# Kernel tuning notes

Measured on AMD Instinct MI355X. Metric: run time of the kernel, lower is better.

## Reference

```python
import jax, jax.numpy as jnp
import numpy as np

B, T, C, HS = 4, 2048, 1024, 64

def setup_inputs() -> dict:
    key = jax.random.key(0)
    k1, k2, k3, k4 = jax.random.split(key, 4)
    x = jax.random.normal(k1, (B, T, C), dtype=jnp.float32)
    # torch Linear default init scale ~ 1/sqrt(fan_in); scale weights similarly
    s = C ** -0.5
    Wq = jax.random.normal(k2, (C, HS), dtype=jnp.float32) * s
    Wk = jax.random.normal(k3, (C, HS), dtype=jnp.float32) * s
    Wv = jax.random.normal(k4, (C, HS), dtype=jnp.float32) * s
    return {"x": x, "Wq": Wq, "Wk": Wk, "Wv": Wv}

def reference(x, Wq, Wk, Wv):
    B_, T_, C_ = x.shape
    q = x @ Wq          # [B,T,HS]
    k = x @ Wk          # [B,T,HS]
    v = x @ Wv          # [B,T,HS]
    scale = C_ ** -0.5  # note: module scales by input dim C, not head_size
    w = jnp.einsum('bqh,bkh->bqk', q, k) * scale  # [B,T,T]
    causal = jnp.tril(jnp.ones((T_, T_), dtype=bool))
    w = jnp.where(causal, w, -jnp.inf)
    a = jax.nn.softmax(w, axis=-1)  # dropout is identity (eval / drop_rate=0)
    return jnp.einsum('bqk,bkh->bqh', a, v)
```

## Files before the change

kernel.cpp:

```cpp
#include <hip/hip_runtime.h>
#include <math.h>

#define B_  4
#define T_  2048
#define C_  1024
#define HS_ 64
#define M_  (B_*T_)
#define NCAT 192
#define SCALE_ 0.03125f
#define XPAD 1032

typedef unsigned short ushort_t;
typedef short bf16x8 __attribute__((ext_vector_type(8)));
typedef float f32x4 __attribute__((ext_vector_type(4)));

static __device__ __forceinline__ unsigned short f2bf(float f) {
    union { float f; unsigned int u; } c; c.f = f;
    unsigned int u = c.u;
    return (unsigned short)((u + 0x7FFFu + ((u >> 16) & 1u)) >> 16);
}
static __device__ __forceinline__ unsigned short f2bf_fast(float f) {
    union { float f; unsigned int u; } c; c.f = f;
    return (unsigned short)((c.u + 0x8000u) >> 16);
}

__global__ void wconv_kernel(const float* __restrict__ Wq, const float* __restrict__ Wk,
                             const float* __restrict__ Wv, ushort_t* __restrict__ wtp) {
    int l = threadIdx.x & 63;
    int g = blockIdx.x * 4 + (threadIdx.x >> 6);
    int c  = g / 12;
    int nt = g % 12;
    const float* W = (nt < 4) ? Wq : (nt < 8) ? Wk : Wv;
    int nn = (nt & 3) * 16 + (l & 15);
    int k0 = c * 32 + (l >> 4) * 8;
    union { bf16x8 v; ushort_t u[8]; } pk;
    #pragma unroll
    for (int e = 0; e < 8; e++)
        pk.u[e] = f2bf(W[(size_t)(k0 + e) * HS_ + nn]);
    *(bf16x8*)(wtp + ((size_t)g * 64 + l) * 8) = pk.v;
}

__global__ __launch_bounds__(512, 4) void proj_kernel(const float* __restrict__ x,
    const ushort_t* __restrict__ wtp,
    ushort_t* __restrict__ qws, ushort_t* __restrict__ kws, ushort_t* __restrict__ vt) {
    __shared__ __align__(16) unsigned char pool[49152];

    int tid  = threadIdx.x;
    int wid  = tid >> 6;
    int lane = tid & 63;
    int qd   = lane >> 4;
    int lq   = lane & 15;
    int r0   = blockIdx.x * 16;

    ushort_t* xs = (ushort_t*)pool;
    {
        float4 xv[8];
        #pragma unroll
        for (int j = 0; j < 8; j++) {
            int flat4 = j * 512 + tid;
            int row   = flat4 >> 8;
            int c4    = flat4 & 255;
            xv[j] = *(const float4*)(x + (size_t)(r0 + row) * C_ + c4 * 4);
        }
        #pragma unroll
        for (int j = 0; j < 8; j++) {
            int flat4 = j * 512 + tid;
            int row   = flat4 >> 8;
            int c4    = flat4 & 255;
            uint2 p;
            p.x = (unsigned)f2bf(xv[j].x) | ((unsigned)f2bf(xv[j].y) << 16);
            p.y = (unsigned)f2bf(xv[j].z) | ((unsigned)f2bf(xv[j].w) << 16);
            *(uint2*)(xs + row * XPAD + c4 * 4) = p;
        }
    }
    __syncthreads();

    f32x4 acc[12];
    #pragma unroll
    for (int i = 0; i < 12; i++) acc[i] = (f32x4){0.f,0.f,0.f,0.f};

    const ushort_t* xrow = xs + lq * XPAD + wid * 128 + qd * 8;
    #pragma unroll
    for (int i = 0; i < 4; i++) {
        bf16x8 af = *(const bf16x8*)(xrow + i * 32);
        #pragma unroll
        for (int nt = 0; nt < 12; nt++) {
            bf16x8 bv = *(const bf16x8*)(wtp +
                (((size_t)(wid * 4 + i) * 12 + nt) * 64 + lane) * 8);
            acc[nt] = __builtin_amdgcn_mfma_f32_16x16x32_bf16(af, bv, acc[nt], 0, 0, 0);
        }
    }

    __syncthreads();
    f32x4 (*red)[12 * 64] = (f32x4 (*)[12 * 64])pool;
    if (wid >= 4) {
        #pragma unroll
        for (int nt = 0; nt < 12; nt++) red[wid - 4][nt * 64 + lane] = acc[nt];
    }
    __syncthreads();
    if (wid < 4) {
        #pragma unroll
        for (int nt = 0; nt < 12; nt++) acc[nt] += red[wid][nt * 64 + lane];
    }
    __syncthreads();
    if (wid == 2 || wid == 3) {
        #pragma unroll
        for (int nt = 0; nt < 12; nt++) red[wid][nt * 64 + lane] = acc[nt];
    }
    __syncthreads();
    if (wid < 2) {
        #pragma unroll
        for (int nt = 0; nt < 12; nt++) acc[nt] += red[wid + 2][nt * 64 + lane];
    }
    __syncthreads();
    if (wid == 1) {
        #pragma unroll
        for (int nt = 0; nt < 12; nt++) red[0][nt * 64 + lane] = acc[nt];
    }
    __syncthreads();
    if (wid == 0) {
        #pragma unroll
        for (int nt = 0; nt < 12; nt++) {
            acc[nt] += red[0][nt * 64 + lane];
            int outn = nt >> 2;
            int col  = (nt & 3) * 16 + lq;
            #pragma unroll
            for (int r = 0; r < 4; r++) {
                int row = r0 + qd * 4 + r;
                float v = acc[nt][r];
                if (outn == 0) v *= SCALE_;
                ushort_t val = f2bf(v);
                if (outn == 0)      qws[(size_t)row * HS_ + col] = val;
                else if (outn == 1) kws[(size_t)row * HS_ + col] = val;
                else {
                    int b = row >> 11, t = row & 2047;
                    vt[((size_t)b * 64 + col) * T_ + t] = val;
                }
            }
        }
    }
}

__global__ __launch_bounds__(512, 2) void flash_kernel(const ushort_t* __restrict__ qws,
    const ushort_t* __restrict__ kws, const ushort_t* __restrict__ vt,
    float* __restrict__ out) {
    __shared__ __align__(16) unsigned char pool[18432];

    int tid  = threadIdx.x;
    int wid  = tid >> 6;
    int lane = tid & 63;
    int qd   = lane >> 4;
    int lq   = lane & 15;
    int ts   = wid >> 2;
    int ws   = wid & 3;

    int batch = blockIdx.y;
    int p     = blockIdx.x;
    int tile  = ts ? (127 - p) : p;
    int q0    = tile * 16;
    int qrow  = q0 + lq;
    int grow  = batch * T_ + qrow;
    int nU    = (tile + 4) >> 2;

    bf16x8 qf[2];
    #pragma unroll
    for (int st = 0; st < 2; st++)
        qf[st] = *(const bf16x8*)(qws + (size_t)grow * HS_ + st * 32 + qd * 8);

    float lsum = 0.f;
    f32x4 O[4];
    #pragma unroll
    for (int nt = 0; nt < 4; nt++) O[nt] = (f32x4){0.f,0.f,0.f,0.f};

    ushort_t* pw = (ushort_t*)pool + wid * 1152 + lq * 72;
    const ushort_t* kp    = kws + (size_t)batch * T_ * HS_;
    const ushort_t* vbase = vt  + (size_t)batch * 64 * T_;

    for (int u = ws; u < nU; u += 4) {
        int kb = u * 64;

        bf16x8 kf[8], vf[8];
        #pragma unroll
        for (int sub = 0; sub < 4; sub++)
            #pragma unroll
            for (int st = 0; st < 2; st++)
                kf[sub * 2 + st] = *(const bf16x8*)(kp + (size_t)(kb + sub * 16 + lq) * HS_ + st * 32 + qd * 8);
        #pragma unroll
        for (int nt = 0; nt < 4; nt++)
            #pragma unroll
            for (int kk = 0; kk < 2; kk++)
                vf[nt * 2 + kk] = *(const bf16x8*)(vbase + ((size_t)nt * 16 + lq) * T_ + kb + kk * 32 + qd * 8);

        f32x4 S[4];
        #pragma unroll
        for (int sub = 0; sub < 4; sub++) {
            f32x4 s = (f32x4){0.f,0.f,0.f,0.f};
            #pragma unroll
            for (int st = 0; st < 2; st++)
                s = __builtin_amdgcn_mfma_f32_16x16x32_bf16(kf[sub * 2 + st], qf[st], s, 0, 0, 0);
            S[sub] = s;
        }

        if (kb + 64 > q0) {
            #pragma unroll
            for (int sub = 0; sub < 4; sub++)
                #pragma unroll
                for (int r = 0; r < 4; r++) {
                    int key = kb + sub * 16 + qd * 4 + r;
                    float pv = (key <= qrow) ? __expf(S[sub][r]) : 0.f;
                    S[sub][r] = pv;
                    lsum += pv;
                }
        } else {
            #pragma unroll
            for (int sub = 0; sub < 4; sub++)
                #pragma unroll
                for (int r = 0; r < 4; r++) {
                    float pv = __expf(S[sub][r]);
                    S[sub][r] = pv;
                    lsum += pv;
                }
        }

        #pragma unroll
        for (int sub = 0; sub < 4; sub++) {
            uint2 d;
            d.x = (unsigned)f2bf_fast(S[sub][0]) | ((unsigned)f2bf_fast(S[sub][1]) << 16);
            d.y = (unsigned)f2bf_fast(S[sub][2]) | ((unsigned)f2bf_fast(S[sub][3]) << 16);
            *(uint2*)(pw + sub * 16 + qd * 4) = d;
        }
        bf16x8 pf0 = *(const bf16x8*)(pw + qd * 8);
        bf16x8 pf1 = *(const bf16x8*)(pw + 32 + qd * 8);

        #pragma unroll
        for (int nt = 0; nt < 4; nt++) {
            O[nt] = __builtin_amdgcn_mfma_f32_16x16x32_bf16(vf[nt * 2 + 0], pf0, O[nt], 0, 0, 0);
            O[nt] = __builtin_amdgcn_mfma_f32_16x16x32_bf16(vf[nt * 2 + 1], pf1, O[nt], 0, 0, 0);
        }
    }

    f32x4* red  = (f32x4*)pool;
    float* lred = (float*)(pool + 16384);
    __syncthreads();
    if (ws >= 2) {
        int sl = ts * 2 + (ws - 2);
        f32x4* rs = red + (size_t)sl * 256;
        #pragma unroll
        for (int nt = 0; nt < 4; nt++) rs[nt * 64 + lane] = O[nt];
        lred[sl * 64 + lane] = lsum;
    }
    __syncthreads();
    if (ws < 2) {
        int sl = ts * 2 + ws;
        f32x4* rs = red + (size_t)sl * 256;
        #pragma unroll
        for (int nt = 0; nt < 4; nt++) O[nt] += rs[nt * 64 + lane];
        lsum += lred[sl * 64 + lane];
    }
    __syncthreads();
    if (ws == 1) {
        int sl = ts * 2;
        f32x4* rs = red + (size_t)sl * 256;
        #pragma unroll
        for (int nt = 0; nt < 4; nt++) rs[nt * 64 + lane] = O[nt];
        lred[sl * 64 + lane] = lsum;
    }
    __syncthreads();
    if (ws == 0) {
        int sl = ts * 2;
        f32x4* rs = red + (size_t)sl * 256;
        #pragma unroll
        for (int nt = 0; nt < 4; nt++) O[nt] += rs[nt * 64 + lane];
        lsum += lred[sl * 64 + lane];
        lsum += __shfl_xor(lsum, 16, 64);
        lsum += __shfl_xor(lsum, 32, 64);
        float li = 1.f / lsum;
        #pragma unroll
        for (int nt = 0; nt < 4; nt++) {
            f32x4 o = O[nt] * li;
            *(f32x4*)(out + (size_t)grow * HS_ + nt * 16 + qd * 4) = o;
        }
    }
}

extern "C" void kernel_launch(void* const* d_in, const int* in_sizes, int n_in,
                              void* d_out, int out_size, void* d_ws, size_t ws_size,
                              hipStream_t stream) {
    const float* x  = (const float*)d_in[0];
    const float* Wq = (const float*)d_in[1];
    const float* Wk = (const float*)d_in[2];
    const float* Wv = (const float*)d_in[3];
    float* out = (float*)d_out;

    ushort_t* wtp = (ushort_t*)d_ws;
    ushort_t* qws = wtp + (size_t)384 * 64 * 8;
    ushort_t* kws = qws + (size_t)M_ * HS_;
    ushort_t* vt  = kws + (size_t)M_ * HS_;

    wconv_kernel<<<96, 256, 0, stream>>>(Wq, Wk, Wv, wtp);
    proj_kernel<<<512, 512, 0, stream>>>(x, wtp, qws, kws, vt);
    flash_kernel<<<dim3(64, 4), 512, 0, stream>>>(qws, kws, vt, out);
}
```

Before: 106.8 us.

## Process 32 rows per projection block, reusing weight fragments across two row tiles

The projection kernel now handles 32 rows per block instead of 16. Each weight fragment loaded from global memory feeds two MFMAs, one per 16-row tile, which halves weight traffic per row. The x tile is staged through shared memory in two halves of 512 columns, and the second half's global loads are issued before the first half's compute so they overlap it. The grid halves to 256 blocks, launch bounds drop to 2 waves per SIMD, and the cross-wave reduction now runs twice. This costs fewer blocks to spread across the GPU and more registers per thread.

```diff
diff --git a/kernel.cpp b/kernel.cpp
--- a/kernel.cpp
+++ b/kernel.cpp
@@ -8,7 +8,7 @@
 #define M_  (B_*T_)
 #define NCAT 192
 #define SCALE_ 0.03125f
-#define XPAD 1032
+#define XP2 520
 
 typedef unsigned short ushort_t;
 typedef short bf16x8 __attribute__((ext_vector_type(8)));
@@ -40,59 +40,9 @@
     *(bf16x8*)(wtp + ((size_t)g * 64 + l) * 8) = pk.v;
 }
 
-__global__ __launch_bounds__(512, 4) void proj_kernel(const float* __restrict__ x,
-    const ushort_t* __restrict__ wtp,
+static __device__ __forceinline__ void reduce_epi(f32x4 (&acc)[12], f32x4 (*red)[12 * 64],
+    int wid, int lane, int qd, int lq, int rowbase,
     ushort_t* __restrict__ qws, ushort_t* __restrict__ kws, ushort_t* __restrict__ vt) {
-    __shared__ __align__(16) unsigned char pool[49152];
-
-    int tid  = threadIdx.x;
-    int wid  = tid >> 6;
-    int lane = tid & 63;
-    int qd   = lane >> 4;
-    int lq   = lane & 15;
-    int r0   = blockIdx.x * 16;
-
-    ushort_t* xs = (ushort_t*)pool;
-    {
-        float4 xv[8];
-        #pragma unroll
-        for (int j = 0; j < 8; j++) {
-            int flat4 = j * 512 + tid;
-            int row   = flat4 >> 8;
-            int c4    = flat4 & 255;
-            xv[j] = *(const float4*)(x + (size_t)(r0 + row) * C_ + c4 * 4);
-        }
-        #pragma unroll
-        for (int j = 0; j < 8; j++) {
-            int flat4 = j * 512 + tid;
-            int row   = flat4 >> 8;
-            int c4    = flat4 & 255;
-            uint2 p;
-            p.x = (unsigned)f2bf(xv[j].x) | ((unsigned)f2bf(xv[j].y) << 16);
-            p.y = (unsigned)f2bf(xv[j].z) | ((unsigned)f2bf(xv[j].w) << 16);
-            *(uint2*)(xs + row * XPAD + c4 * 4) = p;
-        }
-    }
-    __syncthreads();
-
-    f32x4 acc[12];
-    #pragma unroll
-    for (int i = 0; i < 12; i++) acc[i] = (f32x4){0.f,0.f,0.f,0.f};
-
-    const ushort_t* xrow = xs + lq * XPAD + wid * 128 + qd * 8;
-    #pragma unroll
-    for (int i = 0; i < 4; i++) {
-        bf16x8 af = *(const bf16x8*)(xrow + i * 32);
-        #pragma unroll
-        for (int nt = 0; nt < 12; nt++) {
-            bf16x8 bv = *(const bf16x8*)(wtp +
-                (((size_t)(wid * 4 + i) * 12 + nt) * 64 + lane) * 8);
-            acc[nt] = __builtin_amdgcn_mfma_f32_16x16x32_bf16(af, bv, acc[nt], 0, 0, 0);
-        }
-    }
-
-    __syncthreads();
-    f32x4 (*red)[12 * 64] = (f32x4 (*)[12 * 64])pool;
     if (wid >= 4) {
         #pragma unroll
         for (int nt = 0; nt < 12; nt++) red[wid - 4][nt * 64 + lane] = acc[nt];
@@ -126,7 +76,7 @@
             int col  = (nt & 3) * 16 + lq;
             #pragma unroll
             for (int r = 0; r < 4; r++) {
-                int row = r0 + qd * 4 + r;
+                int row = rowbase + qd * 4 + r;
                 float v = acc[nt][r];
                 if (outn == 0) v *= SCALE_;
                 ushort_t val = f2bf(v);
@@ -139,6 +89,87 @@
             }
         }
     }
+    __syncthreads();
+}
+
+__global__ __launch_bounds__(512, 2) void proj_kernel(const float* __restrict__ x,
+    const ushort_t* __restrict__ wtp,
+    ushort_t* __restrict__ qws, ushort_t* __restrict__ kws, ushort_t* __restrict__ vt) {
+    __shared__ __align__(16) unsigned char pool[49152];
+    ushort_t* xs = (ushort_t*)pool;
+
+    int tid  = threadIdx.x;
+    int wid  = tid >> 6;
+    int lane = tid & 63;
+    int qd   = lane >> 4;
+    int lq   = lane & 15;
+    int r0   = blockIdx.x * 32;
+
+    f32x4 acc0[12], acc1[12];
+    #pragma unroll
+    for (int i = 0; i < 12; i++) {
+        acc0[i] = (f32x4){0.f,0.f,0.f,0.f};
+        acc1[i] = (f32x4){0.f,0.f,0.f,0.f};
+    }
+
+    {
+        float4 xv[8];
+        #pragma unroll
+        for (int j = 0; j < 8; j++) {
+            int f4 = j * 512 + tid, row = f4 >> 7, c4 = f4 & 127;
+            xv[j] = *(const float4*)(x + (size_t)(r0 + row) * C_ + c4 * 4);
+        }
+        #pragma unroll
+        for (int j = 0; j < 8; j++) {
+            int f4 = j * 512 + tid, row = f4 >> 7, c4 = f4 & 127;
+            uint2 p;
+            p.x = (unsigned)f2bf(xv[j].x) | ((unsigned)f2bf(xv[j].y) << 16);
+            p.y = (unsigned)f2bf(xv[j].z) | ((unsigned)f2bf(xv[j].w) << 16);
+            *(uint2*)(xs + row * XP2 + c4 * 4) = p;
+        }
+    }
+    float4 yv[8];
+    #pragma unroll
+    for (int j = 0; j < 8; j++) {
+        int f4 = j * 512 + tid, row = f4 >> 7, c4 = f4 & 127;
+        yv[j] = *(const float4*)(x + (size_t)(r0 + row) * C_ + 512 + c4 * 4);
+    }
+    __syncthreads();
+
+    #pragma unroll
+    for (int ph = 0; ph < 2; ph++) {
+        const ushort_t* xr0 = xs + lq * XP2 + wid * 64;
+        const ushort_t* xr1 = xr0 + 16 * XP2;
+        #pragma unroll
+        for (int i2 = 0; i2 < 2; i2++) {
+            bf16x8 a0 = *(const bf16x8*)(xr0 + i2 * 32 + qd * 8);
+            bf16x8 a1 = *(const bf16x8*)(xr1 + i2 * 32 + qd * 8);
+            int g = ph * 16 + wid * 2 + i2;
+            #pragma unroll
+            for (int nt = 0; nt < 12; nt++) {
+                bf16x8 bv = *(const bf16x8*)(wtp + (((size_t)g * 12 + nt) * 64 + lane) * 8);
+                acc0[nt] = __builtin_amdgcn_mfma_f32_16x16x32_bf16(a0, bv, acc0[nt], 0, 0, 0);
+                acc1[nt] = __builtin_amdgcn_mfma_f32_16x16x32_bf16(a1, bv, acc1[nt], 0, 0, 0);
+            }
+        }
+        if (ph == 0) {
+            __syncthreads();
+            #pragma unroll
+            for (int j = 0; j < 8; j++) {
+                int f4 = j * 512 + tid, row = f4 >> 7, c4 = f4 & 127;
+                uint2 p;
+                p.x = (unsigned)f2bf(yv[j].x) | ((unsigned)f2bf(yv[j].y) << 16);
+                p.y = (unsigned)f2bf(yv[j].z) | ((unsigned)f2bf(yv[j].w) << 16);
+                *(uint2*)(xs + row * XP2 + c4 * 4) = p;
+            }
+            __syncthreads();
+        }
+    }
+
+    __syncthreads();
+    f32x4 (*red)[12 * 64] = (f32x4 (*)[12 * 64])pool;
+    reduce_epi(acc0, red, wid, lane, qd, lq, r0,      qws, kws, vt);
+    reduce_epi(acc1, red, wid, lane, qd, lq, r0 + 16, qws, kws, vt);
 }
 
 __global__ __launch_bounds__(512, 2) void flash_kernel(const ushort_t* __restrict__ qws,
@@ -298,6 +329,6 @@
     ushort_t* vt  = kws + (size_t)M_ * HS_;
 
     wconv_kernel<<<96, 256, 0, stream>>>(Wq, Wk, Wv, wtp);
-    proj_kernel<<<512, 512, 0, stream>>>(x, wtp, qws, kws, vt);
+    proj_kernel<<<256, 512, 0, stream>>>(x, wtp, qws, kws, vt);
     flash_kernel<<<dim3(64, 4), 512, 0, stream>>>(qws, kws, vt, out);
 }
```

New measurement: 115.3 us. +8.0%, slower.
